# Performance work log

Measured on AMD Instinct MI355X. Metric: run time of the kernel, lower is better.

Reference implementation:

```python
import jax, jax.numpy as jnp
import numpy as np

B, N, C_IN = 8, 2048, 64
NUM_TERMS, NUM_CHANNELS = 3, 64
LN_EPS = 1e-5


def setup_inputs() -> dict:
    key = jax.random.key(0)
    k1, k2, k3 = jax.random.split(key, 3)
    A = jax.random.normal(k1, (B, N, N), dtype=jnp.float32) / jnp.sqrt(N).astype(jnp.float32)
    X = jax.random.normal(k2, (B, N, C_IN), dtype=jnp.float32)
    # xavier_uniform on h of shape [num_terms+1, num_channels, num_nodes]
    fan_in, fan_out = NUM_CHANNELS, N
    bound = float(np.sqrt(6.0 / (fan_in + fan_out)))
    h = jax.random.uniform(k3, (NUM_TERMS + 1, NUM_CHANNELS, N), dtype=jnp.float32,
                           minval=-bound, maxval=bound)
    gamma = jnp.ones((NUM_CHANNELS,), dtype=jnp.float32)
    beta = jnp.zeros((NUM_CHANNELS,), dtype=jnp.float32)
    return {"A": A, "X": X, "h": h, "gamma": gamma, "beta": beta}


def reference(A, X, h, gamma, beta):
    # Original loops compute: Y[b,n,c] = sum_i h[i,c,n] * (A^i @ sum_ch X[...,ch])[b,n]
    num_terms = h.shape[0] - 1
    Xs = X.sum(axis=-1)  # [B, N] -- inner channel loop collapses to a sum

    def step(p, _):
        p_next = jnp.einsum('bmn,bn->bm', A, p)  # A^i @ Xs
        return p_next, p_next

    _, Ps = jax.lax.scan(step, Xs, None, length=num_terms)  # [T, B, N]
    P = jnp.concatenate([Xs[None], Ps], axis=0)  # [T+1, B, N], P[0] = I @ Xs

    Y = jnp.einsum('icn,ibn->bnc', h, P)  # [B, N, C]

    mean = Y.mean(axis=-1, keepdims=True)
    var = Y.var(axis=-1, keepdims=True)
    Yn = (Y - mean) * jax.lax.rsqrt(var + LN_EPS) * gamma + beta
    return jnp.tanh(Yn)
```

## Files before the change

### kernel.cpp

```cpp
#include <hip/hip_runtime.h>
#include <hip/hip_bf16.h>
#include <hip/hip_fp16.h>
#include <math.h>

#define BB 8
#define NN 2048
#define C_IN 64
#define NCH 64
#define LN_EPS 1e-5f

typedef float f4 __attribute__((ext_vector_type(4)));

__global__ void xsum_kernel(const float* __restrict__ X, float* __restrict__ Xs) {
    int row  = (blockIdx.x * blockDim.x + threadIdx.x) >> 6;
    int lane = threadIdx.x & 63;
    float v = X[(size_t)row * C_IN + lane];
    #pragma unroll
    for (int off = 32; off > 0; off >>= 1)
        v += __shfl_down(v, off, 64);
    if (lane == 0) Xs[row] = v;
}

__global__ __launch_bounds__(256, 4) void matvec_cvt_kernel(
        const float* __restrict__ A,
        const float* __restrict__ pin,
        float* __restrict__ pout,
        __half* __restrict__ A16) {
    __shared__ float4 p4[NN / 4];
    const int b = blockIdx.y;

    const float4* src = (const float4*)(pin + (size_t)b * NN);
    p4[threadIdx.x]       = src[threadIdx.x];
    p4[threadIdx.x + 256] = src[threadIdx.x + 256];
    __syncthreads();

    const int wave = threadIdx.x >> 6;
    const int lane = threadIdx.x & 63;
    const int m0   = blockIdx.x * 16 + wave * 4;
    const float* Ab = A + (size_t)b * NN * NN;

    f4 buf[2][8];
    {
        const f4* r = (const f4*)(Ab + (size_t)m0 * NN);
        #pragma unroll
        for (int j = 0; j < 8; ++j)
            buf[0][j] = __builtin_nontemporal_load(&r[j * 64 + lane]);
    }

    #pragma unroll
    for (int i = 0; i < 4; ++i) {
        const int m = m0 + i;
        if (i < 3) {
            const f4* rn = (const f4*)(Ab + (size_t)(m + 1) * NN);
            #pragma unroll
            for (int j = 0; j < 8; ++j)
                buf[(i + 1) & 1][j] = __builtin_nontemporal_load(&rn[j * 64 + lane]);
        }

        float acc = 0.f;
        #pragma unroll
        for (int j = 0; j < 8; ++j) {
            f4 x      = buf[i & 1][j];
            float4 pv = p4[j * 64 + lane];
            acc += x.x * pv.x + x.y * pv.y + x.z * pv.z + x.w * pv.w;
        }

        float2* A16r = (float2*)(A16 + (size_t)b * NN * NN + (size_t)m * NN);
        #pragma unroll
        for (int j = 0; j < 8; ++j) {
            union { float2 f2; __half2 h2[2]; } u;
            u.h2[0] = __floats2half2_rn(buf[i & 1][j].x, buf[i & 1][j].y);
            u.h2[1] = __floats2half2_rn(buf[i & 1][j].z, buf[i & 1][j].w);
            A16r[j * 64 + lane] = u.f2;
        }

        #pragma unroll
        for (int off = 32; off > 0; off >>= 1)
            acc += __shfl_down(acc, off, 64);
        if (lane == 0) pout[(size_t)b * NN + m] = acc;
    }
}

__global__ __launch_bounds__(256, 4) void matvec16_kernel(
        const __half* __restrict__ A16,
        const float* __restrict__ pin,
        float* __restrict__ pout) {
    __shared__ float4 p4[NN / 4];
    const int b = blockIdx.y;

    const float4* src = (const float4*)(pin + (size_t)b * NN);
    p4[threadIdx.x]       = src[threadIdx.x];
    p4[threadIdx.x + 256] = src[threadIdx.x + 256];
    __syncthreads();

    const int wave = threadIdx.x >> 6;
    const int lane = threadIdx.x & 63;
    const int m0   = blockIdx.x * 16 + wave * 4;
    const __half* Ab = A16 + (size_t)b * NN * NN;

    float4 buf[2][4];
    {
        const float4* r = (const float4*)(Ab + (size_t)m0 * NN);
        #pragma unroll
        for (int j = 0; j < 4; ++j) buf[0][j] = r[j * 64 + lane];
    }

    #pragma unroll
    for (int i = 0; i < 4; ++i) {
        const int m = m0 + i;
        if (i < 3) {
            const float4* rn = (const float4*)(Ab + (size_t)(m + 1) * NN);
            #pragma unroll
            for (int j = 0; j < 4; ++j) buf[(i + 1) & 1][j] = rn[j * 64 + lane];
        }

        float acc = 0.f;
        #pragma unroll
        for (int j = 0; j < 4; ++j) {
            float4 pa = p4[2 * (j * 64 + lane)];
            float4 pb = p4[2 * (j * 64 + lane) + 1];
            const __half2* hx = (const __half2*)&buf[i & 1][j];
            float2 f0 = __half22float2(hx[0]);
            float2 f1 = __half22float2(hx[1]);
            float2 f2 = __half22float2(hx[2]);
            float2 f3 = __half22float2(hx[3]);
            acc += f0.x * pa.x + f0.y * pa.y + f1.x * pa.z + f1.y * pa.w
                 + f2.x * pb.x + f2.y * pb.y + f3.x * pb.z + f3.y * pb.w;
        }

        #pragma unroll
        for (int off = 32; off > 0; off >>= 1)
            acc += __shfl_down(acc, off, 64);
        if (lane == 0) pout[(size_t)b * NN + m] = acc;
    }
}

__global__ __launch_bounds__(256, 4) void matvec16_ln_kernel(
        const __half* __restrict__ A16,
        const float* __restrict__ P,
        const float* __restrict__ h,
        const float* __restrict__ gamma,
        const float* __restrict__ beta,
        float* __restrict__ out) {
    __shared__ float4 p4[NN / 4];
    const int b = blockIdx.y;

    const float4* src = (const float4*)(P + (size_t)(2 * BB + b) * NN);
    p4[threadIdx.x]       = src[threadIdx.x];
    p4[threadIdx.x + 256] = src[threadIdx.x + 256];
    __syncthreads();

    const int wave = threadIdx.x >> 6;
    const int lane = threadIdx.x & 63;
    const int m0   = blockIdx.x * 16 + wave * 4;
    const __half* Ab = A16 + (size_t)b * NN * NN;

    float4 buf[2][4];
    {
        const float4* r = (const float4*)(Ab + (size_t)m0 * NN);
        #pragma unroll
        for (int j = 0; j < 4; ++j) buf[0][j] = r[j * 64 + lane];
    }

    #pragma unroll
    for (int i = 0; i < 4; ++i) {
        const int m = m0 + i;
        if (i < 3) {
            const float4* rn = (const float4*)(Ab + (size_t)(m + 1) * NN);
            #pragma unroll
            for (int j = 0; j < 4; ++j) buf[(i + 1) & 1][j] = rn[j * 64 + lane];
        }

        float acc = 0.f;
        #pragma unroll
        for (int j = 0; j < 4; ++j) {
            float4 pa = p4[2 * (j * 64 + lane)];
            float4 pb = p4[2 * (j * 64 + lane) + 1];
            const __half2* hx = (const __half2*)&buf[i & 1][j];
            float2 f0 = __half22float2(hx[0]);
            float2 f1 = __half22float2(hx[1]);
            float2 f2 = __half22float2(hx[2]);
            float2 f3 = __half22float2(hx[3]);
            acc += f0.x * pa.x + f0.y * pa.y + f1.x * pa.z + f1.y * pa.w
                 + f2.x * pb.x + f2.y * pb.y + f3.x * pb.z + f3.y * pb.w;
        }
        #pragma unroll
        for (int off = 32; off > 0; off >>= 1)
            acc += __shfl_xor(acc, off, 64);
        const float p3 = acc;

        const int idx = b * NN + m;
        const float p0 = P[idx];
        const float p1 = P[BB * NN + idx];
        const float p2 = ((const float*)p4)[m & (NN - 1)];

        float y = h[(size_t)(0 * NCH + lane) * NN + m] * p0
                + h[(size_t)(1 * NCH + lane) * NN + m] * p1
                + h[(size_t)(2 * NCH + lane) * NN + m] * p2
                + h[(size_t)(3 * NCH + lane) * NN + m] * p3;

        float s = y;
        #pragma unroll
        for (int off = 32; off > 0; off >>= 1)
            s += __shfl_xor(s, off, 64);
        const float mean = s * (1.f / NCH);

        float d = y - mean;
        float vs = d * d;
        #pragma unroll
        for (int off = 32; off > 0; off >>= 1)
            vs += __shfl_xor(vs, off, 64);
        const float rstd = rsqrtf(vs * (1.f / NCH) + LN_EPS);

        __builtin_nontemporal_store(
            tanhf(d * rstd * gamma[lane] + beta[lane]),
            &out[(size_t)idx * NCH + lane]);
    }
}

extern "C" void kernel_launch(void* const* d_in, const int* in_sizes, int n_in,
                              void* d_out, int out_size, void* d_ws, size_t ws_size,
                              hipStream_t stream) {
    const float* A     = (const float*)d_in[0];
    const float* X     = (const float*)d_in[1];
    const float* h     = (const float*)d_in[2];
    const float* gamma = (const float*)d_in[3];
    const float* beta  = (const float*)d_in[4];
    float* out = (float*)d_out;

    float*  P   = (float*)d_ws;
    __half* A16 = (__half*)((char*)d_ws + (1u << 20));

    dim3 mv_grid(NN / 16, BB);

    xsum_kernel<<<(BB * NN) / 4, 256, 0, stream>>>(X, P);

    matvec_cvt_kernel<<<mv_grid, 256, 0, stream>>>(A, P, P + BB * NN, A16);

    matvec16_kernel<<<mv_grid, 256, 0, stream>>>(
        A16, P + BB * NN, P + 2 * BB * NN);

    matvec16_ln_kernel<<<mv_grid, 256, 0, stream>>>(
        A16, P, h, gamma, beta, out);
}
```

Baseline: 237.6 us.

## Fuse all stages into one persistent kernel with software grid barriers

Replaces the four separate launches (channel sum, fp32 matvec plus fp16 conversion, fp16 matvec, fp16 matvec plus LayerNorm) with a single kernel of 512 blocks that synchronise through an atomic-counter grid barrier, reset each call by a memset. Each block now handles 32 rows instead of 16. The final stage stages h into shared memory in a transposed layout so the four term weights for a node are read with one vector load, instead of four strided global loads. This removes launch gaps and tail effects between stages, but it depends on all 512 blocks being co-resident, and the barrier spin has a guard that exits silently on timeout. It also adds a memset and serialises the grid at each barrier.

Result: slower. 389.8 us (+64.0%).

```diff
diff --git a/kernel.cpp b/kernel.cpp
--- a/kernel.cpp
+++ b/kernel.cpp
@@ -1,220 +1,245 @@
 #include <hip/hip_runtime.h>
-#include <hip/hip_bf16.h>
 #include <hip/hip_fp16.h>
 #include <math.h>
 
 #define BB 8
 #define NN 2048
-#define C_IN 64
 #define NCH 64
 #define LN_EPS 1e-5f
+#define BN (BB * NN)
+#define NBLK 512
 
 typedef float f4 __attribute__((ext_vector_type(4)));
 
-__global__ void xsum_kernel(const float* __restrict__ X, float* __restrict__ Xs) {
-    int row  = (blockIdx.x * blockDim.x + threadIdx.x) >> 6;
-    int lane = threadIdx.x & 63;
-    float v = X[(size_t)row * C_IN + lane];
-    #pragma unroll
-    for (int off = 32; off > 0; off >>= 1)
-        v += __shfl_down(v, off, 64);
-    if (lane == 0) Xs[row] = v;
+__device__ __forceinline__ void grid_barrier(unsigned* bar, unsigned target) {
+    __syncthreads();
+    if (threadIdx.x == 0) {
+        __threadfence();
+        __hip_atomic_fetch_add(bar, 1u, __ATOMIC_ACQ_REL, __HIP_MEMORY_SCOPE_AGENT);
+        int guard = 0;
+        while (__hip_atomic_load(bar, __ATOMIC_ACQUIRE, __HIP_MEMORY_SCOPE_AGENT) < target) {
+            __builtin_amdgcn_s_sleep(2);
+            if (++guard > (1 << 20)) break;
+        }
+        __threadfence();
+    }
+    __syncthreads();
 }
 
-__global__ __launch_bounds__(256, 4) void matvec_cvt_kernel(
+__global__ __launch_bounds__(256, 2) void fused_all(
         const float* __restrict__ A,
-        const float* __restrict__ pin,
-        float* __restrict__ pout,
-        __half* __restrict__ A16) {
-    __shared__ float4 p4[NN / 4];
-    const int b = blockIdx.y;
-
-    const float4* src = (const float4*)(pin + (size_t)b * NN);
-    p4[threadIdx.x]       = src[threadIdx.x];
-    p4[threadIdx.x + 256] = src[threadIdx.x + 256];
-    __syncthreads();
-
-    const int wave = threadIdx.x >> 6;
-    const int lane = threadIdx.x & 63;
-    const int m0   = blockIdx.x * 16 + wave * 4;
-    const float* Ab = A + (size_t)b * NN * NN;
-
-    f4 buf[2][8];
-    {
-        const f4* r = (const f4*)(Ab + (size_t)m0 * NN);
-        #pragma unroll
-        for (int j = 0; j < 8; ++j)
-            buf[0][j] = __builtin_nontemporal_load(&r[j * 64 + lane]);
-    }
-
-    #pragma unroll
-    for (int i = 0; i < 4; ++i) {
-        const int m = m0 + i;
-        if (i < 3) {
-            const f4* rn = (const f4*)(Ab + (size_t)(m + 1) * NN);
-            #pragma unroll
-            for (int j = 0; j < 8; ++j)
-                buf[(i + 1) & 1][j] = __builtin_nontemporal_load(&rn[j * 64 + lane]);
-        }
-
-        float acc = 0.f;
-        #pragma unroll
-        for (int j = 0; j < 8; ++j) {
-            f4 x      = buf[i & 1][j];
-            float4 pv = p4[j * 64 + lane];
-            acc += x.x * pv.x + x.y * pv.y + x.z * pv.z + x.w * pv.w;
-        }
-
-        float2* A16r = (float2*)(A16 + (size_t)b * NN * NN + (size_t)m * NN);
-        #pragma unroll
-        for (int j = 0; j < 8; ++j) {
-            union { float2 f2; __half2 h2[2]; } u;
-            u.h2[0] = __floats2half2_rn(buf[i & 1][j].x, buf[i & 1][j].y);
-            u.h2[1] = __floats2half2_rn(buf[i & 1][j].z, buf[i & 1][j].w);
-            A16r[j * 64 + lane] = u.f2;
-        }
-
-        #pragma unroll
-        for (int off = 32; off > 0; off >>= 1)
-            acc += __shfl_down(acc, off, 64);
-        if (lane == 0) pout[(size_t)b * NN + m] = acc;
-    }
-}
-
-__global__ __launch_bounds__(256, 4) void matvec16_kernel(
-        const __half* __restrict__ A16,
-        const float* __restrict__ pin,
-        float* __restrict__ pout) {
-    __shared__ float4 p4[NN / 4];
-    const int b = blockIdx.y;
-
-    const float4* src = (const float4*)(pin + (size_t)b * NN);
-    p4[threadIdx.x]       = src[threadIdx.x];
-    p4[threadIdx.x + 256] = src[threadIdx.x + 256];
-    __syncthreads();
-
-    const int wave = threadIdx.x >> 6;
-    const int lane = threadIdx.x & 63;
-    const int m0   = blockIdx.x * 16 + wave * 4;
-    const __half* Ab = A16 + (size_t)b * NN * NN;
-
-    float4 buf[2][4];
-    {
-        const float4* r = (const float4*)(Ab + (size_t)m0 * NN);
-        #pragma unroll
-        for (int j = 0; j < 4; ++j) buf[0][j] = r[j * 64 + lane];
-    }
-
-    #pragma unroll
-    for (int i = 0; i < 4; ++i) {
-        const int m = m0 + i;
-        if (i < 3) {
-            const float4* rn = (const float4*)(Ab + (size_t)(m + 1) * NN);
-            #pragma unroll
-            for (int j = 0; j < 4; ++j) buf[(i + 1) & 1][j] = rn[j * 64 + lane];
-        }
-
-        float acc = 0.f;
-        #pragma unroll
-        for (int j = 0; j < 4; ++j) {
-            float4 pa = p4[2 * (j * 64 + lane)];
-            float4 pb = p4[2 * (j * 64 + lane) + 1];
-            const __half2* hx = (const __half2*)&buf[i & 1][j];
-            float2 f0 = __half22float2(hx[0]);
-            float2 f1 = __half22float2(hx[1]);
-            float2 f2 = __half22float2(hx[2]);
-            float2 f3 = __half22float2(hx[3]);
-            acc += f0.x * pa.x + f0.y * pa.y + f1.x * pa.z + f1.y * pa.w
-                 + f2.x * pb.x + f2.y * pb.y + f3.x * pb.z + f3.y * pb.w;
-        }
-
-        #pragma unroll
-        for (int off = 32; off > 0; off >>= 1)
-            acc += __shfl_down(acc, off, 64);
-        if (lane == 0) pout[(size_t)b * NN + m] = acc;
-    }
-}
-
-__global__ __launch_bounds__(256, 4) void matvec16_ln_kernel(
-        const __half* __restrict__ A16,
-        const float* __restrict__ P,
+        const float* __restrict__ X,
         const float* __restrict__ h,
         const float* __restrict__ gamma,
         const float* __restrict__ beta,
-        float* __restrict__ out) {
+        float* __restrict__ out,
+        float* __restrict__ P,
+        __half* __restrict__ A16,
+        unsigned* __restrict__ bar) {
     __shared__ float4 p4[NN / 4];
-    const int b = blockIdx.y;
-
-    const float4* src = (const float4*)(P + (size_t)(2 * BB + b) * NN);
-    p4[threadIdx.x]       = src[threadIdx.x];
-    p4[threadIdx.x + 256] = src[threadIdx.x + 256];
-    __syncthreads();
-
-    const int wave = threadIdx.x >> 6;
-    const int lane = threadIdx.x & 63;
-    const int m0   = blockIdx.x * 16 + wave * 4;
-    const __half* Ab = A16 + (size_t)b * NN * NN;
-
-    float4 buf[2][4];
+    __shared__ float  hs[32][NCH][4];
+
+    const int tid  = threadIdx.x;
+    const int wave = tid >> 6;
+    const int lane = tid & 63;
+    const int blk  = blockIdx.x;
+    const int b    = blk >> 6;
+    const int bx   = blk & 63;
+
+    #pragma unroll
+    for (int s = 0; s < 2; ++s) {
+        const int row = blk * 32 + s * 16 + (tid >> 4);
+        const int q   = tid & 15;
+        float4 x = ((const float4*)X)[(size_t)row * 16 + q];
+        float v = x.x + x.y + x.z + x.w;
+        v += __shfl_xor(v, 8, 64);
+        v += __shfl_xor(v, 4, 64);
+        v += __shfl_xor(v, 2, 64);
+        v += __shfl_xor(v, 1, 64);
+        if (q == 0) P[row] = v;
+    }
+    grid_barrier(bar, NBLK);
+
     {
-        const float4* r = (const float4*)(Ab + (size_t)m0 * NN);
+        const float4* src = (const float4*)(P + (size_t)b * NN);
+        p4[tid]       = src[tid];
+        p4[tid + 256] = src[tid + 256];
+        __syncthreads();
+
+        const float* Ab = A + (size_t)b * NN * NN;
         #pragma unroll
-        for (int j = 0; j < 4; ++j) buf[0][j] = r[j * 64 + lane];
-    }
-
-    #pragma unroll
-    for (int i = 0; i < 4; ++i) {
-        const int m = m0 + i;
-        if (i < 3) {
-            const float4* rn = (const float4*)(Ab + (size_t)(m + 1) * NN);
-            #pragma unroll
-            for (int j = 0; j < 4; ++j) buf[(i + 1) & 1][j] = rn[j * 64 + lane];
-        }
-
-        float acc = 0.f;
+        for (int s = 0; s < 2; ++s) {
+            const int m0 = bx * 32 + s * 16 + wave * 4;
+            f4 buf[2][8];
+            {
+                const f4* r = (const f4*)(Ab + (size_t)m0 * NN);
+                #pragma unroll
+                for (int j = 0; j < 8; ++j)
+                    buf[0][j] = __builtin_nontemporal_load(&r[j * 64 + lane]);
+            }
+            #pragma unroll
+            for (int i = 0; i < 4; ++i) {
+                const int m = m0 + i;
+                if (i < 3) {
+                    const f4* rn = (const f4*)(Ab + (size_t)(m + 1) * NN);
+                    #pragma unroll
+                    for (int j = 0; j < 8; ++j)
+                        buf[(i + 1) & 1][j] = __builtin_nontemporal_load(&rn[j * 64 + lane]);
+                }
+                float acc = 0.f;
+                #pragma unroll
+                for (int j = 0; j < 8; ++j) {
+                    f4 x      = buf[i & 1][j];
+                    float4 pv = p4[j * 64 + lane];
+                    acc += x.x * pv.x + x.y * pv.y + x.z * pv.z + x.w * pv.w;
+                }
+                float2* A16r = (float2*)(A16 + (size_t)b * NN * NN + (size_t)m * NN);
+                #pragma unroll
+                for (int j = 0; j < 8; ++j) {
+                    union { float2 f2; __half2 h2[2]; } u;
+                    u.h2[0] = __floats2half2_rn(buf[i & 1][j].x, buf[i & 1][j].y);
+                    u.h2[1] = __floats2half2_rn(buf[i & 1][j].z, buf[i & 1][j].w);
+                    A16r[j * 64 + lane] = u.f2;
+                }
+                #pragma unroll
+                for (int off = 32; off > 0; off >>= 1)
+                    acc += __shfl_down(acc, off, 64);
+                if (lane == 0) P[BN + (size_t)b * NN + m] = acc;
+            }
+        }
+    }
+    grid_barrier(bar, 2 * NBLK);
+
+    {
+        const float4* src = (const float4*)(P + BN + (size_t)b * NN);
+        p4[tid]       = src[tid];
+        p4[tid + 256] = src[tid + 256];
+        __syncthreads();
+
+        const __half* Ab = A16 + (size_t)b * NN * NN;
         #pragma unroll
-        for (int j = 0; j < 4; ++j) {
-            float4 pa = p4[2 * (j * 64 + lane)];
-            float4 pb = p4[2 * (j * 64 + lane) + 1];
-            const __half2* hx = (const __half2*)&buf[i & 1][j];
-            float2 f0 = __half22float2(hx[0]);
-            float2 f1 = __half22float2(hx[1]);
-            float2 f2 = __half22float2(hx[2]);
-            float2 f3 = __half22float2(hx[3]);
-            acc += f0.x * pa.x + f0.y * pa.y + f1.x * pa.z + f1.y * pa.w
-                 + f2.x * pb.x + f2.y * pb.y + f3.x * pb.z + f3.y * pb.w;
-        }
+        for (int s = 0; s < 2; ++s) {
+            const int m0 = bx * 32 + s * 16 + wave * 4;
+            float4 buf[2][4];
+            {
+                const float4* r = (const float4*)(Ab + (size_t)m0 * NN);
+                #pragma unroll
+                for (int j = 0; j < 4; ++j) buf[0][j] = r[j * 64 + lane];
+            }
+            #pragma unroll
+            for (int i = 0; i < 4; ++i) {
+                const int m = m0 + i;
+                if (i < 3) {
+                    const float4* rn = (const float4*)(Ab + (size_t)(m + 1) * NN);
+                    #pragma unroll
+                    for (int j = 0; j < 4; ++j) buf[(i + 1) & 1][j] = rn[j * 64 + lane];
+                }
+                float acc = 0.f;
+                #pragma unroll
+                for (int j = 0; j < 4; ++j) {
+                    float4 pa = p4[2 * (j * 64 + lane)];
+                    float4 pb = p4[2 * (j * 64 + lane) + 1];
+                    const __half2* hx = (const __half2*)&buf[i & 1][j];
+                    float2 f0 = __half22float2(hx[0]);
+                    float2 f1 = __half22float2(hx[1]);
+                    float2 f2 = __half22float2(hx[2]);
+                    float2 f3 = __half22float2(hx[3]);
+                    acc += f0.x * pa.x + f0.y * pa.y + f1.x * pa.z + f1.y * pa.w
+                         + f2.x * pb.x + f2.y * pb.y + f3.x * pb.z + f3.y * pb.w;
+                }
+                #pragma unroll
+                for (int off = 32; off > 0; off >>= 1)
+                    acc += __shfl_down(acc, off, 64);
+                if (lane == 0) P[2 * BN + (size_t)b * NN + m] = acc;
+            }
+        }
+    }
+    grid_barrier(bar, 3 * NBLK);
+
+    {
+        const float4* src = (const float4*)(P + 2 * BN + (size_t)b * NN);
+        p4[tid]       = src[tid];
+        p4[tid + 256] = src[tid + 256];
+
+        {
+            const float4* hr =
+                (const float4*)(h + ((size_t)(wave * NCH + lane)) * NN + bx * 32);
+            #pragma unroll
+            for (int k = 0; k < 8; ++k) {
+                float4 hv = hr[k];
+                hs[k * 4 + 0][lane][wave] = hv.x;
+                hs[k * 4 + 1][lane][wave] = hv.y;
+                hs[k * 4 + 2][lane][wave] = hv.z;
+                hs[k * 4 + 3][lane][wave] = hv.w;
+            }
+        }
+        __syncthreads();
+
+        const float g  = gamma[lane];
+        const float be = beta[lane];
+        const __half* Ab = A16 + (size_t)b * NN * NN;
         #pragma unroll
-        for (int off = 32; off > 0; off >>= 1)
-            acc += __shfl_xor(acc, off, 64);
-        const float p3 = acc;
-
-        const int idx = b * NN + m;
-        const float p0 = P[idx];
-        const float p1 = P[BB * NN + idx];
-        const float p2 = ((const float*)p4)[m & (NN - 1)];
-
-        float y = h[(size_t)(0 * NCH + lane) * NN + m] * p0
-                + h[(size_t)(1 * NCH + lane) * NN + m] * p1
-                + h[(size_t)(2 * NCH + lane) * NN + m] * p2
-                + h[(size_t)(3 * NCH + lane) * NN + m] * p3;
-
-        float s = y;
-        #pragma unroll
-        for (int off = 32; off > 0; off >>= 1)
-            s += __shfl_xor(s, off, 64);
-        const float mean = s * (1.f / NCH);
-
-        float d = y - mean;
-        float vs = d * d;
-        #pragma unroll
-        for (int off = 32; off > 0; off >>= 1)
-            vs += __shfl_xor(vs, off, 64);
-        const float rstd = rsqrtf(vs * (1.f / NCH) + LN_EPS);
-
-        __builtin_nontemporal_store(
-            tanhf(d * rstd * gamma[lane] + beta[lane]),
-            &out[(size_t)idx * NCH + lane]);
+        for (int s = 0; s < 2; ++s) {
+            const int m0 = bx * 32 + s * 16 + wave * 4;
+            float4 buf[2][4];
+            {
+                const float4* r = (const float4*)(Ab + (size_t)m0 * NN);
+                #pragma unroll
+                for (int j = 0; j < 4; ++j) buf[0][j] = r[j * 64 + lane];
+            }
+            #pragma unroll
+            for (int i = 0; i < 4; ++i) {
+                const int m = m0 + i;
+                if (i < 3) {
+                    const float4* rn = (const float4*)(Ab + (size_t)(m + 1) * NN);
+                    #pragma unroll
+                    for (int j = 0; j < 4; ++j) buf[(i + 1) & 1][j] = rn[j * 64 + lane];
+                }
+                const int idx  = b * NN + m;
+                const float p0 = P[idx];
+                const float p1 = P[BN + idx];
+
+                float acc = 0.f;
+                #pragma unroll
+                for (int j = 0; j < 4; ++j) {
+                    float4 pa = p4[2 * (j * 64 + lane)];
+                    float4 pb = p4[2 * (j * 64 + lane) + 1];
+                    const __half2* hx = (const __half2*)&buf[i & 1][j];
+                    float2 f0 = __half22float2(hx[0]);
+                    float2 f1 = __half22float2(hx[1]);
+                    float2 f2 = __half22float2(hx[2]);
+                    float2 f3 = __half22float2(hx[3]);
+                    acc += f0.x * pa.x + f0.y * pa.y + f1.x * pa.z + f1.y * pa.w
+                         + f2.x * pb.x + f2.y * pb.y + f3.x * pb.z + f3.y * pb.w;
+                }
+                #pragma unroll
+                for (int off = 32; off > 0; off >>= 1)
+                    acc += __shfl_xor(acc, off, 64);
+                const float p3 = acc;
+                const float p2 = ((const float*)p4)[m];
+
+                const int  node = s * 16 + wave * 4 + i;
+                const float4 hv = *(const float4*)&hs[node][lane][0];
+                float y = hv.x * p0 + hv.y * p1 + hv.z * p2 + hv.w * p3;
+
+                float sum = y;
+                #pragma unroll
+                for (int off = 32; off > 0; off >>= 1)
+                    sum += __shfl_xor(sum, off, 64);
+                const float mean = sum * (1.f / NCH);
+
+                float d  = y - mean;
+                float vs = d * d;
+                #pragma unroll
+                for (int off = 32; off > 0; off >>= 1)
+                    vs += __shfl_xor(vs, off, 64);
+                const float rstd = rsqrtf(vs * (1.f / NCH) + LN_EPS);
+
+                __builtin_nontemporal_store(
+                    tanhf(d * rstd * g + be),
+                    &out[(size_t)idx * NCH + lane]);
+            }
+        }
     }
 }
 
@@ -228,18 +253,12 @@
     const float* beta  = (const float*)d_in[4];
     float* out = (float*)d_out;
 
-    float*  P   = (float*)d_ws;
-    __half* A16 = (__half*)((char*)d_ws + (1u << 20));
-
-    dim3 mv_grid(NN / 16, BB);
-
-    xsum_kernel<<<(BB * NN) / 4, 256, 0, stream>>>(X, P);
-
-    matvec_cvt_kernel<<<mv_grid, 256, 0, stream>>>(A, P, P + BB * NN, A16);
-
-    matvec16_kernel<<<mv_grid, 256, 0, stream>>>(
-        A16, P + BB * NN, P + 2 * BB * NN);
-
-    matvec16_ln_kernel<<<mv_grid, 256, 0, stream>>>(
-        A16, P, h, gamma, beta, out);
+    unsigned* bar = (unsigned*)d_ws;
+    float*    P   = (float*)((char*)d_ws + 4096);
+    __half*   A16 = (__half*)((char*)d_ws + (1u << 20));
+
+    hipMemsetAsync(d_ws, 0, 256, stream);
+
+    fused_all<<<dim3(NBLK), dim3(256), 0, stream>>>(
+        A, X, h, gamma, beta, out, P, A16, bar);
 }
```
